# Performance work log

Measured on AMD Instinct MI355X. Metric: run time of the kernel, lower is better.

Reference implementation:

```python
import jax, jax.numpy as jnp
import numpy as np


def setup_inputs() -> dict:
    key = jax.random.key(0)
    ks = jax.random.split(key, 6)
    b, c, h, w = 8, 256, 48, 48
    return {
        "qry_fts": jax.random.normal(ks[0], (b, c, h, w), dtype=jnp.float32),
        "mask_fts": jax.random.normal(ks[1], (b, c, h, w), dtype=jnp.float32),
        "fts": jax.random.normal(ks[2], (b, c, h, w), dtype=jnp.float32),
        "Wq": jax.random.normal(ks[3], (c, c), dtype=jnp.float32) * (1.0 / np.sqrt(c)),
        "Wk": jax.random.normal(ks[4], (c, c), dtype=jnp.float32) * (1.0 / np.sqrt(c)),
        "Wv": jax.random.normal(ks[5], (c, c), dtype=jnp.float32) * (1.0 / np.sqrt(c)),
        "mu": jnp.full((1,), 0.5, dtype=jnp.float32),
    }


def reference(qry_fts, mask_fts, fts, Wq, Wk, Wv, mu):
    b, c, h, w = qry_fts.shape
    # flatten spatial dims to tokens: [b, N, c], N = h*w
    q_tok = qry_fts.reshape(b, c, h * w).transpose(0, 2, 1)
    m_tok = mask_fts.reshape(b, c, h * w).transpose(0, 2, 1)
    f_tok = fts.reshape(b, c, h * w).transpose(0, 2, 1)

    # torch Linear(no bias): y = x @ W^T with W [out,in]
    Q = jnp.einsum("bnc,dc->bnd", q_tok, Wq)
    K1 = jnp.einsum("bnc,dc->bnd", f_tok, Wk)
    K2 = jnp.einsum("bnc,dc->bnd", m_tok, Wk)
    V = jnp.einsum("bnc,dc->bnd", f_tok, Wv)

    A1 = jax.nn.softmax(jnp.einsum("bqd,bkd->bqk", Q, K1), axis=-1)
    A2 = jax.nn.softmax(jnp.einsum("bqd,bkd->bqk", Q, K2), axis=-1)
    A = (A1 * 0.5 + A2 * mu[0]) / (0.5 + mu[0])

    att = jnp.einsum("bqk,bkd->bqd", A, V)  # [b, N, c]
    att = att.reshape(b, h, w, c).transpose(0, 3, 1, 2)
    return qry_fts + att
```

## Files before the change

### kernel.cpp

```cpp
#include <hip/hip_runtime.h>
#include <math.h>

#define BB 8
#define CC 256
#define NTOK 2304
#define NPL 36
#define LOG2E 1.4426950408889634f
#define BIAS2 72.134752f

typedef __attribute__((ext_vector_type(4))) float f32x4;
typedef __attribute__((ext_vector_type(8))) short s16x8;
typedef __attribute__((ext_vector_type(4))) short s16x4;

__device__ inline unsigned short f2bf(float x) {
  unsigned u = __builtin_bit_cast(unsigned, x);
  return (unsigned short)((u + 0x7FFFu + ((u >> 16) & 1u)) >> 16);
}
__device__ inline float bf2f(unsigned short h) {
  return __builtin_bit_cast(float, (unsigned)h << 16);
}
__device__ inline unsigned short f2h(float x) {
  _Float16 h = (_Float16)x;
  return __builtin_bit_cast(unsigned short, h);
}

__device__ inline void async16(void* lds, const void* g) {
  __builtin_amdgcn_global_load_lds(
      (const __attribute__((address_space(1))) unsigned int*)g,
      (__attribute__((address_space(3))) unsigned int*)lds, 16, 0, 0);
}

__global__ __launch_bounds__(256)
void prep_kernel(const float* __restrict__ X0, const float* __restrict__ X1,
                 const float* __restrict__ X2, unsigned short* __restrict__ Y0,
                 unsigned short* __restrict__ Y1, unsigned short* __restrict__ Y2,
                 const float* __restrict__ W0, const float* __restrict__ W1,
                 const float* __restrict__ W2, unsigned short* __restrict__ Wh0,
                 unsigned short* __restrict__ Wh1, unsigned short* __restrict__ Wh2) {
  __shared__ float Ls[64][65];
  const int t = threadIdx.x;
  const int z = blockIdx.z;

  if (z == 24) {
    int idx = (blockIdx.x * 4 + blockIdx.y) * 256 + t;
    for (int e = idx; e < 49152; e += 36864) {
      int m = e / 16384, r = e - m * 16384;
      const float* s = (m == 0) ? W0 : (m == 1) ? W1 : W2;
      unsigned short* d = (m == 0) ? Wh0 : (m == 1) ? Wh1 : Wh2;
      f32x4 v = *(const f32x4*)(s + r * 4);
      s16x4 o;
      #pragma unroll
      for (int i = 0; i < 4; i++) o[i] = (short)f2h(v[i]);
      *(s16x4*)(d + r * 4) = o;
    }
    return;
  }

  const int n0 = blockIdx.x * 64, c0 = blockIdx.y * 64;
  const int src = z >> 3, b = z & 7;
  const float* X = (src == 0) ? X0 : (src == 1) ? X1 : X2;
  unsigned short* Y = (src == 0) ? Y0 : (src == 1) ? Y1 : Y2;
  const float* Xb = X + (size_t)b * CC * NTOK;
  unsigned short* Yb = Y + (size_t)b * CC * NTOK;

  #pragma unroll
  for (int rr = 0; rr < 16; rr++) {
    int cl = rr * 4 + (t >> 6);
    Ls[cl][t & 63] = Xb[(size_t)(c0 + cl) * NTOK + n0 + (t & 63)];
  }
  __syncthreads();
  #pragma unroll
  for (int rr = 0; rr < 8; rr++) {
    int nl = rr * 8 + (t >> 5);
    int cl = (t & 31) * 2;
    unsigned v = (unsigned)f2h(Ls[cl][nl]) | ((unsigned)f2h(Ls[cl + 1][nl]) << 16);
    *(unsigned*)((char*)Yb + ((size_t)(n0 + nl) * CC + c0 + cl) * 2) = v;
  }
}

__global__ __launch_bounds__(256, 2)
void gemm_kernel(const unsigned short* __restrict__ Xtq, const unsigned short* __restrict__ Xtm,
                 const unsigned short* __restrict__ Xtf, const unsigned short* __restrict__ Wqh,
                 const unsigned short* __restrict__ Wkh, const unsigned short* __restrict__ Wvh,
                 unsigned short* __restrict__ Qw, unsigned short* __restrict__ K1w,
                 unsigned short* __restrict__ K2w, unsigned short* __restrict__ Vtw) {
  __shared__ alignas(16) char smem[32768];

  const int m = blockIdx.y;
  const unsigned short* Xt = (m == 0) ? Xtq : (m == 2) ? Xtm : Xtf;
  const unsigned short* Wh = (m == 0) ? Wqh : (m == 3) ? Wvh : Wkh;
  unsigned short* Y = (m == 0) ? Qw : (m == 1) ? K1w : (m == 2) ? K2w : Vtw;

  const int t = threadIdx.x;
  const int w = t >> 6, l = t & 63, g = l >> 4, c = l & 15;
  const int bid = blockIdx.x;
  const int b = bid & 7, nt = bid >> 3;
  const int n0w = nt * 64 + w * 16;
  const size_t bo = (size_t)b * CC * NTOK;

  const char* Xb = (const char*)(Xt + bo);
  const char* Wb = (const char*)Wh;
  char* Yb = (char*)(Y + bo);

  int koff[4], cdst[4];
  #pragma unroll
  for (int j = 0; j < 4; j++) {
    int ck = w + 4 * j;
    int row = ck * 2 + (l >> 5);
    koff[j] = row * 512 + (((l & 31) * 16) ^ ((row & 7) << 4));
    cdst[j] = ck * 1024 + l * 16;
  }
  int kxor[8];
  #pragma unroll
  for (int dc = 0; dc < 8; dc++)
    kxor[dc] = (dc * 64 + g * 16) ^ ((c & 7) << 4);

  s16x8 xa[8];
  #pragma unroll
  for (int dc = 0; dc < 8; dc++)
    xa[dc] = *(const s16x8*)(Xb + (n0w + c) * 512 + dc * 64 + g * 16);

  f32x4 acc[16];

#define STAGE_W(WB, TILE)                                            \
  do {                                                               \
    _Pragma("unroll")                                                \
    for (int j_ = 0; j_ < 4; j_++)                                   \
      async16((WB) + cdst[j_], Wb + (TILE) * 16384 + koff[j_]);      \
  } while (0)

  STAGE_W(smem, 0);
  __syncthreads();

  #pragma unroll
  for (int ph = 0; ph < 8; ph++) {
    char* cur = smem + (ph & 1) * 16384;
    if (ph < 7) STAGE_W(smem + ((ph & 1) ^ 1) * 16384, ph + 1);
    __builtin_amdgcn_s_setprio(1);
    #pragma unroll
    for (int s = 0; s < 2; s++) {
      const char* Kt = cur + (s * 16 + c) * 512;
      f32x4 sx[2] = {(f32x4){0.f, 0.f, 0.f, 0.f}, (f32x4){0.f, 0.f, 0.f, 0.f}};
      #pragma unroll
      for (int dc = 0; dc < 8; dc++) {
        s16x8 wf = *(const s16x8*)(Kt + kxor[dc]);
        sx[dc >> 2] = __builtin_amdgcn_mfma_f32_16x16x32_f16(xa[dc], wf, sx[dc >> 2], 0, 0, 0);
      }
      acc[ph * 2 + s] = sx[0] + sx[1];
    }
    __builtin_amdgcn_s_setprio(0);
    __syncthreads();
  }
#undef STAGE_W

  if (m != 3) {
    unsigned short* Ws = (unsigned short*)(smem + w * 8192);
    const float scale = (m == 0) ? LOG2E : 1.0f;
    #pragma unroll
    for (int dt = 0; dt < 16; dt++)
      #pragma unroll
      for (int j = 0; j < 4; j++)
        Ws[(g * 4 + j) * 256 + dt * 16 + c] = f2h(acc[dt][j] * scale);
    #pragma unroll
    for (int r = 0; r < 16; r++) {
      s16x4 v = *(const s16x4*)&Ws[r * 256 + l * 4];
      *(s16x4*)(Yb + (size_t)(n0w + r) * 512 + l * 8) = v;
    }
  } else {
    unsigned short* Vs = (unsigned short*)(smem + w * 8192);
    #pragma unroll
    for (int dt = 0; dt < 16; dt++) {
      s16x4 pv;
      #pragma unroll
      for (int j = 0; j < 4; j++) pv[j] = (short)f2bf(acc[dt][j]);
      *(s16x4*)&Vs[c * 20 + g * 4] = pv;
      s16x4 vv = *(const s16x4*)&Vs[(l >> 2) * 20 + (l & 3) * 4];
      *(s16x4*)(Yb + (size_t)(dt * 16 + (l >> 2)) * 4608 + (size_t)(n0w + (l & 3) * 4) * 2) = vv;
    }
  }
}

__global__ __launch_bounds__(256, 2)
void attn_kernel(const unsigned short* __restrict__ Qf, const unsigned short* __restrict__ K1,
                 const unsigned short* __restrict__ K2, const unsigned short* __restrict__ Vt,
                 unsigned short* __restrict__ pa1, unsigned short* __restrict__ pa2,
                 float* __restrict__ lb) {
  __shared__ alignas(16) char smem[77824];
  char* const kb0 = smem;
  char* const kb1 = smem + 16384;

  const int t = threadIdx.x;
  const int w = t >> 6, l = t & 63, g = l >> 4, c = l & 15;
  const int path = w >> 1, qs = w & 1;
  const int bid = blockIdx.x;
  const int b = bid & 7;
  const int r0 = bid >> 3;
  const int qt = r0 % 36, half = r0 / 36;
  const int q0 = qt * 64 + qs * 32;
  const size_t bo = (size_t)b * CC * NTOK;

  const char* Qb  = (const char*)(Qf + bo);
  const char* K1b = (const char*)(K1 + bo);
  const char* K2b = (const char*)(K2 + bo);
  const char* Vtb = (const char*)(Vt + bo);

  unsigned short* const Pe  = (unsigned short*)(smem + 65536 + w * 3072);
  unsigned short* const Pod = Pe + 768;

  int koff[2], voff[2], cdst[2];
  #pragma unroll
  for (int j = 0; j < 2; j++) {
    int ck = w + 4 * j;
    int tok = ck * 2 + (l >> 5);
    koff[j] = tok * 512 + (((l & 31) * 16) ^ ((tok & 7) << 4));
    voff[j] = (ck * 32 + (l >> 1)) * 4608 + (((l & 1) ^ ((l >> 3) & 1)) << 4);
    cdst[j] = ck * 1024 + l * 16;
  }

  int kxor[8];
  #pragma unroll
  for (int dc = 0; dc < 8; dc++)
    kxor[dc] = (dc * 64 + g * 16) ^ ((c & 7) << 4);

  s16x8 qf[2][8];
  #pragma unroll
  for (int st = 0; st < 2; st++)
    #pragma unroll
    for (int dc = 0; dc < 8; dc++)
      qf[st][dc] = *(const s16x8*)(Qb + (q0 + st * 16 + c) * 512 + dc * 64 + g * 16);

  f32x4 a0[16], a1r[16];
  #pragma unroll
  for (int dt = 0; dt < 16; dt++) {
    a0[dt]  = (f32x4){0.f, 0.f, 0.f, 0.f};
    a1r[dt] = (f32x4){0.f, 0.f, 0.f, 0.f};
  }
  float lr[2][4] = {{0.f, 0.f, 0.f, 0.f}, {0.f, 0.f, 0.f, 0.f}};

#define STAGE_K(KB, TILE)                                                  \
  do {                                                                     \
    _Pragma("unroll")                                                      \
    for (int pp_ = 0; pp_ < 2; pp_++) {                                    \
      const char* ks_ = (pp_ ? K2b : K1b) + (size_t)(TILE) * 8192;         \
      async16((KB) + pp_ * 8192 + cdst[0], ks_ + koff[0]);                 \
      async16((KB) + pp_ * 8192 + cdst[1], ks_ + koff[1]);                 \
    }                                                                      \
  } while (0)

#define STAGE_V(VB, PAIR)                                                  \
  do {                                                                     \
    _Pragma("unroll")                                                      \
    for (int h_ = 0; h_ < 2; h_++) {                                       \
      const char* vs_ = Vtb + (PAIR) * 64 + h_ * 32;                       \
      async16((VB) + h_ * 8192 + cdst[0], vs_ + voff[0]);                  \
      async16((VB) + h_ * 8192 + cdst[1], vs_ + voff[1]);                  \
    }                                                                      \
  } while (0)

  const int tb = half * 72;
  const int pb = half * 36;

  STAGE_K(kb0, tb);
  STAGE_V(smem + 32768, pb);
  __syncthreads();

  for (int p = 0; p < NPL; p++) {
    char* vcur = smem + 32768 + (p & 1) * 16384;
    char* vnxt = smem + 32768 + ((p & 1) ^ 1) * 16384;

    STAGE_K(kb1, tb + 2 * p + 1);
    {
      const char* Kt = kb0 + path * 8192 + c * 512;
      f32x4 s0 = (f32x4){0.f, 0.f, 0.f, 0.f};
      f32x4 s1 = (f32x4){0.f, 0.f, 0.f, 0.f};
      __builtin_amdgcn_s_setprio(1);
      #pragma unroll
      for (int dc = 0; dc < 8; dc++) {
        s16x8 kf = *(const s16x8*)(Kt + kxor[dc]);
        s0 = __builtin_amdgcn_mfma_f32_16x16x32_f16(qf[0][dc], kf, s0, 0, 0, 0);
        s1 = __builtin_amdgcn_mfma_f32_16x16x32_f16(qf[1][dc], kf, s1, 0, 0, 0);
      }
      __builtin_amdgcn_s_setprio(0);
      #pragma unroll
      for (int j = 0; j < 4; j++) {
        float pv = exp2f(s0[j] - BIAS2);
        lr[0][j] += pv;
        Pe[(g * 4 + j) * 24 + c] = f2bf(pv);
        float pw = exp2f(s1[j] - BIAS2);
        lr[1][j] += pw;
        Pe[(16 + g * 4 + j) * 24 + c] = f2bf(pw);
      }
    }
    __syncthreads();

    if (p + 1 < NPL) {
      STAGE_K(kb0, tb + 2 * p + 2);
      STAGE_V(vnxt, pb + p + 1);
    }
    {
      const char* Kt = kb1 + path * 8192 + c * 512;
      f32x4 s0 = (f32x4){0.f, 0.f, 0.f, 0.f};
      f32x4 s1 = (f32x4){0.f, 0.f, 0.f, 0.f};
      __builtin_amdgcn_s_setprio(1);
      #pragma unroll
      for (int dc = 0; dc < 8; dc++) {
        s16x8 kf = *(const s16x8*)(Kt + kxor[dc]);
        s0 = __builtin_amdgcn_mfma_f32_16x16x32_f16(qf[0][dc], kf, s0, 0, 0, 0);
        s1 = __builtin_amdgcn_mfma_f32_16x16x32_f16(qf[1][dc], kf, s1, 0, 0, 0);
      }
      __builtin_amdgcn_s_setprio(0);
      #pragma unroll
      for (int j = 0; j < 4; j++) {
        float pv = exp2f(s0[j] - BIAS2);
        lr[0][j] += pv;
        Pod[(g * 4 + j) * 24 + c] = f2bf(pv);
        float pw = exp2f(s1[j] - BIAS2);
        lr[1][j] += pw;
        Pod[(16 + g * 4 + j) * 24 + c] = f2bf(pw);
      }
    }
    {
      s16x8 pa0 = *(const s16x8*)(((g < 2) ? Pe : Pod) + (c) * 24 + (g & 1) * 8);
      s16x8 pa1 = *(const s16x8*)(((g < 2) ? Pe : Pod) + (16 + c) * 24 + (g & 1) * 8);
      const char* vbase = vcur + ((g >= 2) ? 8192 : 0) + c * 32 +
                          ((((g & 1) ^ ((c >> 2) & 1))) << 4);
      __builtin_amdgcn_s_setprio(1);
      #pragma unroll
      for (int dt = 0; dt < 16; dt++) {
        s16x8 vf = *(const s16x8*)(vbase + dt * 512);
        a0[dt]  = __builtin_amdgcn_mfma_f32_16x16x32_bf16(pa0, vf, a0[dt], 0, 0, 0);
        a1r[dt] = __builtin_amdgcn_mfma_f32_16x16x32_bf16(pa1, vf, a1r[dt], 0, 0, 0);
      }
      __builtin_amdgcn_s_setprio(0);
    }
    __syncthreads();
  }
#undef STAGE_K
#undef STAGE_V

  #pragma unroll
  for (int st = 0; st < 2; st++)
    #pragma unroll
    for (int j = 0; j < 4; j++) {
      #pragma unroll
      for (int off = 1; off < 16; off <<= 1)
        lr[st][j] += __shfl_xor(lr[st][j], off);
    }
  const int pqidx = (half * 8 + b) * 36 + qt;
  if (c == 0) {
    #pragma unroll
    for (int st = 0; st < 2; st++)
      #pragma unroll
      for (int j = 0; j < 4; j++)
        lb[path * 36864 + pqidx * 64 + qs * 32 + st * 16 + g * 4 + j] = lr[st][j];
  }

  unsigned short* const pdst = (path ? pa2 : pa1) + (size_t)pqidx * 16384;
  float* Ws = (float*)(smem + w * 4352);
  const int q = l & 15, ds = l >> 4;
  #pragma unroll
  for (int st = 0; st < 2; st++) {
    const f32x4* ap = st ? a1r : a0;
    #pragma unroll
    for (int ch = 0; ch < 4; ch++) {
      #pragma unroll
      for (int dtp = 0; dtp < 4; dtp++) {
        const int dt = ch * 4 + dtp;
        #pragma unroll
        for (int j = 0; j < 4; j++)
          Ws[(g * 4 + j) * 68 + dtp * 16 + c] = ap[dt][j];
      }
      #pragma unroll
      for (int i = 0; i < 16; i++) {
        int d = ch * 64 + i * 4 + ds;
        pdst[d * 64 + qs * 32 + st * 16 + q] = f2bf(Ws[q * 68 + i * 4 + ds]);
      }
    }
  }
}

__global__ __launch_bounds__(256)
void combine_kernel(const unsigned short* __restrict__ pa1, const unsigned short* __restrict__ pa2,
                    const float* __restrict__ lb, const float* __restrict__ qry,
                    const float* __restrict__ mup, float* __restrict__ out) {
  const int bid = blockIdx.x;
  const int dh = blockIdx.y;
  const int b = bid & 7, qt = bid >> 3;
  const int t = threadIdx.x;
  const int q = t & 63, dr = t >> 6;
  const size_t bo = (size_t)b * CC * NTOK;
  const int q0 = qt * 64;

  const int i0 = (0 * 8 + b) * 36 + qt;
  const int i1 = (1 * 8 + b) * 36 + qt;
  float l1 = lb[i0 * 64 + q] + lb[i1 * 64 + q];
  float l2 = lb[36864 + i0 * 64 + q] + lb[36864 + i1 * 64 + q];
  const float mu = mup[0];
  const float w1 = 0.5f / (0.5f + mu) / l1;
  const float w2 = mu / (0.5f + mu) / l2;

  const unsigned short* p10 = pa1 + (size_t)i0 * 16384;
  const unsigned short* p11 = pa1 + (size_t)i1 * 16384;
  const unsigned short* p20 = pa2 + (size_t)i0 * 16384;
  const unsigned short* p21 = pa2 + (size_t)i1 * 16384;

  #pragma unroll
  for (int i = 0; i < 32; i++) {
    int d = dh * 128 + dr * 32 + i;
    int off = d * 64 + q;
    float av1 = bf2f(p10[off]) + bf2f(p11[off]);
    float av2 = bf2f(p20[off]) + bf2f(p21[off]);
    size_t gi = bo + (size_t)d * NTOK + q0 + q;
    out[gi] = qry[gi] + av1 * w1 + av2 * w2;
  }
}

extern "C" void kernel_launch(void* const* d_in, const int* in_sizes, int n_in,
                              void* d_out, int out_size, void* d_ws, size_t ws_size,
                              hipStream_t stream) {
  const float* qry  = (const float*)d_in[0];
  const float* mask = (const float*)d_in[1];
  const float* fts  = (const float*)d_in[2];
  const float* Wq   = (const float*)d_in[3];
  const float* Wk   = (const float*)d_in[4];
  const float* Wv   = (const float*)d_in[5];
  const float* mu   = (const float*)d_in[6];
  float* out = (float*)d_out;

  const size_t SZ = (size_t)BB * CC * NTOK;
  unsigned short* base = (unsigned short*)d_ws;
  unsigned short* PA1 = base;
  unsigned short* PA2 = base + 9437184;
  float*          LB  = (float*)(base + 18874368);
  unsigned short* Xtq = base;
  unsigned short* Xtm = base + SZ;
  unsigned short* Xtf = base + 2 * SZ;
  unsigned short* Qw  = base + 19169280;
  unsigned short* K1w = Qw + SZ;
  unsigned short* K2w = Qw + 2 * SZ;
  unsigned short* Vtw = Qw + 3 * SZ;
  unsigned short* Wqh = Qw + 4 * SZ;
  unsigned short* Wkh = Wqh + CC * CC;
  unsigned short* Wvh = Wkh + CC * CC;

  prep_kernel<<<dim3(NTOK / 64, CC / 64, 25), 256, 0, stream>>>(
      qry, mask, fts, Xtq, Xtm, Xtf, Wq, Wk, Wv, Wqh, Wkh, Wvh);

  const int GG = BB * (NTOK / 64);
  gemm_kernel<<<dim3(GG, 4), 256, 0, stream>>>(Xtq, Xtm, Xtf, Wqh, Wkh, Wvh,
                                               Qw, K1w, K2w, Vtw);

  attn_kernel<<<2 * GG, 256, 0, stream>>>(Qw, K1w, K2w, Vtw, PA1, PA2, LB);
  combine_kernel<<<dim3(GG, 2), 256, 0, stream>>>(PA1, PA2, LB, qry, mu, out);
}
```

Measured before the change: 226.9 us.

## Split attention block into eight waves of sixteen queries each

The attention kernel now launches 512 threads per block, so each of 8 waves handles 16 query rows instead of 32. This halves the per-wave accumulator and Q-fragment registers, and each thread issues one async copy per K/V half instead of two. The aim is more resident waves to hide latency. In exchange, K and V fragments are read from shared memory once per 16 queries rather than once per 32, roughly doubling LDS read traffic per useful MFMA.

```diff
diff --git a/kernel.cpp b/kernel.cpp
--- a/kernel.cpp
+++ b/kernel.cpp
@@ -180,7 +180,7 @@
   }
 }
 
-__global__ __launch_bounds__(256, 2)
+__global__ __launch_bounds__(512, 4)
 void attn_kernel(const unsigned short* __restrict__ Qf, const unsigned short* __restrict__ K1,
                  const unsigned short* __restrict__ K2, const unsigned short* __restrict__ Vt,
                  unsigned short* __restrict__ pa1, unsigned short* __restrict__ pa2,
@@ -191,12 +191,12 @@
 
   const int t = threadIdx.x;
   const int w = t >> 6, l = t & 63, g = l >> 4, c = l & 15;
-  const int path = w >> 1, qs = w & 1;
+  const int path = w >> 2, qs = w & 3;
   const int bid = blockIdx.x;
   const int b = bid & 7;
   const int r0 = bid >> 3;
   const int qt = r0 % 36, half = r0 / 36;
-  const int q0 = qt * 64 + qs * 32;
+  const int q0 = qt * 64 + qs * 16;
   const size_t bo = (size_t)b * CC * NTOK;
 
   const char* Qb  = (const char*)(Qf + bo);
@@ -204,57 +204,42 @@
   const char* K2b = (const char*)(K2 + bo);
   const char* Vtb = (const char*)(Vt + bo);
 
-  unsigned short* const Pe  = (unsigned short*)(smem + 65536 + w * 3072);
-  unsigned short* const Pod = Pe + 768;
-
-  int koff[2], voff[2], cdst[2];
-  #pragma unroll
-  for (int j = 0; j < 2; j++) {
-    int ck = w + 4 * j;
-    int tok = ck * 2 + (l >> 5);
-    koff[j] = tok * 512 + (((l & 31) * 16) ^ ((tok & 7) << 4));
-    voff[j] = (ck * 32 + (l >> 1)) * 4608 + (((l & 1) ^ ((l >> 3) & 1)) << 4);
-    cdst[j] = ck * 1024 + l * 16;
-  }
+  unsigned short* const Pe  = (unsigned short*)(smem + 65536 + w * 1536);
+  unsigned short* const Pod = Pe + 384;
+
+  const int rid = w * 64 + l;
+  const int ktok = rid >> 5;
+  const int koff = ktok * 512 + (((rid & 31) * 16) ^ ((ktok & 7) << 4));
+  const int vrow = rid >> 1;
+  const int voff = vrow * 4608 + 16 * ((rid & 1) ^ ((rid >> 3) & 1));
+  const int cdst = rid * 16;
 
   int kxor[8];
   #pragma unroll
   for (int dc = 0; dc < 8; dc++)
     kxor[dc] = (dc * 64 + g * 16) ^ ((c & 7) << 4);
 
-  s16x8 qf[2][8];
-  #pragma unroll
-  for (int st = 0; st < 2; st++)
-    #pragma unroll
-    for (int dc = 0; dc < 8; dc++)
-      qf[st][dc] = *(const s16x8*)(Qb + (q0 + st * 16 + c) * 512 + dc * 64 + g * 16);
-
-  f32x4 a0[16], a1r[16];
-  #pragma unroll
-  for (int dt = 0; dt < 16; dt++) {
-    a0[dt]  = (f32x4){0.f, 0.f, 0.f, 0.f};
-    a1r[dt] = (f32x4){0.f, 0.f, 0.f, 0.f};
-  }
-  float lr[2][4] = {{0.f, 0.f, 0.f, 0.f}, {0.f, 0.f, 0.f, 0.f}};
+  s16x8 qf[8];
+  #pragma unroll
+  for (int dc = 0; dc < 8; dc++)
+    qf[dc] = *(const s16x8*)(Qb + (q0 + c) * 512 + dc * 64 + g * 16);
+
+  f32x4 acc[16];
+  #pragma unroll
+  for (int dt = 0; dt < 16; dt++)
+    acc[dt] = (f32x4){0.f, 0.f, 0.f, 0.f};
+  float lr[4] = {0.f, 0.f, 0.f, 0.f};
 
 #define STAGE_K(KB, TILE)                                                  \
   do {                                                                     \
-    _Pragma("unroll")                                                      \
-    for (int pp_ = 0; pp_ < 2; pp_++) {                                    \
-      const char* ks_ = (pp_ ? K2b : K1b) + (size_t)(TILE) * 8192;         \
-      async16((KB) + pp_ * 8192 + cdst[0], ks_ + koff[0]);                 \
-      async16((KB) + pp_ * 8192 + cdst[1], ks_ + koff[1]);                 \
-    }                                                                      \
+    async16((KB) + cdst, K1b + (size_t)(TILE) * 8192 + koff);              \
+    async16((KB) + 8192 + cdst, K2b + (size_t)(TILE) * 8192 + koff);       \
   } while (0)
 
 #define STAGE_V(VB, PAIR)                                                  \
   do {                                                                     \
-    _Pragma("unroll")                                                      \
-    for (int h_ = 0; h_ < 2; h_++) {                                       \
-      const char* vs_ = Vtb + (PAIR) * 64 + h_ * 32;                       \
-      async16((VB) + h_ * 8192 + cdst[0], vs_ + voff[0]);                  \
-      async16((VB) + h_ * 8192 + cdst[1], vs_ + voff[1]);                  \
-    }                                                                      \
+    async16((VB) + cdst, Vtb + (size_t)(PAIR) * 64 + voff);                \
+    async16((VB) + 8192 + cdst, Vtb + (size_t)(PAIR) * 64 + 32 + voff);    \
   } while (0)
 
   const int tb = half * 72;
@@ -271,24 +256,22 @@
     STAGE_K(kb1, tb + 2 * p + 1);
     {
       const char* Kt = kb0 + path * 8192 + c * 512;
-      f32x4 s0 = (f32x4){0.f, 0.f, 0.f, 0.f};
-      f32x4 s1 = (f32x4){0.f, 0.f, 0.f, 0.f};
+      f32x4 sx0 = (f32x4){0.f, 0.f, 0.f, 0.f};
+      f32x4 sx1 = (f32x4){0.f, 0.f, 0.f, 0.f};
       __builtin_amdgcn_s_setprio(1);
       #pragma unroll
       for (int dc = 0; dc < 8; dc++) {
         s16x8 kf = *(const s16x8*)(Kt + kxor[dc]);
-        s0 = __builtin_amdgcn_mfma_f32_16x16x32_f16(qf[0][dc], kf, s0, 0, 0, 0);
-        s1 = __builtin_amdgcn_mfma_f32_16x16x32_f16(qf[1][dc], kf, s1, 0, 0, 0);
+        if (dc < 4) sx0 = __builtin_amdgcn_mfma_f32_16x16x32_f16(qf[dc], kf, sx0, 0, 0, 0);
+        else        sx1 = __builtin_amdgcn_mfma_f32_16x16x32_f16(qf[dc], kf, sx1, 0, 0, 0);
       }
       __builtin_amdgcn_s_setprio(0);
+      f32x4 s = sx0 + sx1;
       #pragma unroll
       for (int j = 0; j < 4; j++) {
-        float pv = exp2f(s0[j] - BIAS2);
-        lr[0][j] += pv;
+        float pv = exp2f(s[j] - BIAS2);
+        lr[j] += pv;
         Pe[(g * 4 + j) * 24 + c] = f2bf(pv);
-        float pw = exp2f(s1[j] - BIAS2);
-        lr[1][j] += pw;
-        Pe[(16 + g * 4 + j) * 24 + c] = f2bf(pw);
       }
     }
     __syncthreads();
@@ -299,37 +282,33 @@
     }
     {
       const char* Kt = kb1 + path * 8192 + c * 512;
-      f32x4 s0 = (f32x4){0.f, 0.f, 0.f, 0.f};
-      f32x4 s1 = (f32x4){0.f, 0.f, 0.f, 0.f};
+      f32x4 sx0 = (f32x4){0.f, 0.f, 0.f, 0.f};
+      f32x4 sx1 = (f32x4){0.f, 0.f, 0.f, 0.f};
       __builtin_amdgcn_s_setprio(1);
       #pragma unroll
       for (int dc = 0; dc < 8; dc++) {
         s16x8 kf = *(const s16x8*)(Kt + kxor[dc]);
-        s0 = __builtin_amdgcn_mfma_f32_16x16x32_f16(qf[0][dc], kf, s0, 0, 0, 0);
-        s1 = __builtin_amdgcn_mfma_f32_16x16x32_f16(qf[1][dc], kf, s1, 0, 0, 0);
+        if (dc < 4) sx0 = __builtin_amdgcn_mfma_f32_16x16x32_f16(qf[dc], kf, sx0, 0, 0, 0);
+        else        sx1 = __builtin_amdgcn_mfma_f32_16x16x32_f16(qf[dc], kf, sx1, 0, 0, 0);
       }
       __builtin_amdgcn_s_setprio(0);
+      f32x4 s = sx0 + sx1;
       #pragma unroll
       for (int j = 0; j < 4; j++) {
-        float pv = exp2f(s0[j] - BIAS2);
-        lr[0][j] += pv;
+        float pv = exp2f(s[j] - BIAS2);
+        lr[j] += pv;
         Pod[(g * 4 + j) * 24 + c] = f2bf(pv);
-        float pw = exp2f(s1[j] - BIAS2);
-        lr[1][j] += pw;
-        Pod[(16 + g * 4 + j) * 24 + c] = f2bf(pw);
       }
     }
     {
-      s16x8 pa0 = *(const s16x8*)(((g < 2) ? Pe : Pod) + (c) * 24 + (g & 1) * 8);
-      s16x8 pa1 = *(const s16x8*)(((g < 2) ? Pe : Pod) + (16 + c) * 24 + (g & 1) * 8);
+      s16x8 pa = *(const s16x8*)(((g < 2) ? Pe : Pod) + c * 24 + (g & 1) * 8);
       const char* vbase = vcur + ((g >= 2) ? 8192 : 0) + c * 32 +
                           ((((g & 1) ^ ((c >> 2) & 1))) << 4);
       __builtin_amdgcn_s_setprio(1);
       #pragma unroll
       for (int dt = 0; dt < 16; dt++) {
         s16x8 vf = *(const s16x8*)(vbase + dt * 512);
-        a0[dt]  = __builtin_amdgcn_mfma_f32_16x16x32_bf16(pa0, vf, a0[dt], 0, 0, 0);
-        a1r[dt] = __builtin_amdgcn_mfma_f32_16x16x32_bf16(pa1, vf, a1r[dt], 0, 0, 0);
+        acc[dt] = __builtin_amdgcn_mfma_f32_16x16x32_bf16(pa, vf, acc[dt], 0, 0, 0);
       }
       __builtin_amdgcn_s_setprio(0);
     }
@@ -339,42 +318,34 @@
 #undef STAGE_V
 
   #pragma unroll
-  for (int st = 0; st < 2; st++)
-    #pragma unroll
-    for (int j = 0; j < 4; j++) {
-      #pragma unroll
-      for (int off = 1; off < 16; off <<= 1)
-        lr[st][j] += __shfl_xor(lr[st][j], off);
-    }
+  for (int j = 0; j < 4; j++) {
+    #pragma unroll
+    for (int off = 1; off < 16; off <<= 1)
+      lr[j] += __shfl_xor(lr[j], off);
+  }
   const int pqidx = (half * 8 + b) * 36 + qt;
   if (c == 0) {
     #pragma unroll
-    for (int st = 0; st < 2; st++)
-      #pragma unroll
-      for (int j = 0; j < 4; j++)
-        lb[path * 36864 + pqidx * 64 + qs * 32 + st * 16 + g * 4 + j] = lr[st][j];
+    for (int j = 0; j < 4; j++)
+      lb[path * 36864 + pqidx * 64 + qs * 16 + g * 4 + j] = lr[j];
   }
 
   unsigned short* const pdst = (path ? pa2 : pa1) + (size_t)pqidx * 16384;
   float* Ws = (float*)(smem + w * 4352);
   const int q = l & 15, ds = l >> 4;
   #pragma unroll
-  for (int st = 0; st < 2; st++) {
-    const f32x4* ap = st ? a1r : a0;
-    #pragma unroll
-    for (int ch = 0; ch < 4; ch++) {
-      #pragma unroll
-      for (int dtp = 0; dtp < 4; dtp++) {
-        const int dt = ch * 4 + dtp;
-        #pragma unroll
-        for (int j = 0; j < 4; j++)
-          Ws[(g * 4 + j) * 68 + dtp * 16 + c] = ap[dt][j];
-      }
-      #pragma unroll
-      for (int i = 0; i < 16; i++) {
-        int d = ch * 64 + i * 4 + ds;
-        pdst[d * 64 + qs * 32 + st * 16 + q] = f2bf(Ws[q * 68 + i * 4 + ds]);
-      }
+  for (int ch = 0; ch < 4; ch++) {
+    #pragma unroll
+    for (int dtp = 0; dtp < 4; dtp++) {
+      const int dt = ch * 4 + dtp;
+      #pragma unroll
+      for (int j = 0; j < 4; j++)
+        Ws[(g * 4 + j) * 68 + dtp * 16 + c] = acc[dt][j];
+    }
+    #pragma unroll
+    for (int i = 0; i < 16; i++) {
+      int d = ch * 64 + i * 4 + ds;
+      pdst[d * 64 + qs * 16 + q] = f2bf(Ws[q * 68 + i * 4 + ds]);
     }
   }
 }
@@ -450,6 +421,6 @@
   gemm_kernel<<<dim3(GG, 4), 256, 0, stream>>>(Xtq, Xtm, Xtf, Wqh, Wkh, Wvh,
                                                Qw, K1w, K2w, Vtw);
 
-  attn_kernel<<<2 * GG, 256, 0, stream>>>(Qw, K1w, K2w, Vtw, PA1, PA2, LB);
+  attn_kernel<<<2 * GG, 512, 0, stream>>>(Qw, K1w, K2w, Vtw, PA1, PA2, LB);
   combine_kernel<<<dim3(GG, 2), 256, 0, stream>>>(PA1, PA2, LB, qry, mu, out);
 }
```

New measurement: 426.1 us. 87.8% more time.
